# Performance work log

Measured on AMD Instinct MI355X. Metric: run time of the kernel, lower is better.

## Reference

```python
import jax, jax.numpy as jnp
import numpy as np

N = 50000      # nodes
E = 800000     # edges
FEAT = 128     # node_feat_size
HID = 128      # hidden_channels
LAT = 64       # latent_size
G = 256        # number of graphs in the batch


def _glorot_like(key, fan_in, shape):
    s = 1.0 / np.sqrt(fan_in)
    return jax.random.uniform(key, shape, jnp.float32, -s, s)


def setup_inputs() -> dict:
    key = jax.random.key(0)
    ks = jax.random.split(key, 13)
    x = jax.random.normal(ks[0], (N, FEAT), jnp.float32)
    edge_index = jax.random.randint(ks[1], (2, E), 0, N, dtype=jnp.int64)
    batch = jnp.sort(jax.random.randint(ks[2], (N,), 0, G, dtype=jnp.int64))
    return {
        "x": x,
        "edge_index": edge_index,
        "batch": batch,
        # GCNConv1: FEAT -> HID
        "W1": _glorot_like(ks[3], FEAT, (FEAT, HID)), "b1": jnp.zeros((HID,), jnp.float32),
        # GCNConv2: HID -> HID
        "W2": _glorot_like(ks[4], HID, (HID, HID)), "b2": jnp.zeros((HID,), jnp.float32),
        # fc: HID -> LAT
        "fcW": _glorot_like(ks[5], HID, (HID, LAT)), "fcb": _glorot_like(ks[6], HID, (LAT,)),
        # decoder: LAT -> HID
        "decW": _glorot_like(ks[7], LAT, (LAT, HID)), "decb": _glorot_like(ks[8], LAT, (HID,)),
        # GCNConv3: HID -> FEAT
        "W3": _glorot_like(ks[9], HID, (HID, FEAT)), "b3": jnp.zeros((FEAT,), jnp.float32),
    }


def reference(x, edge_index, batch, W1, b1, W2, b2, fcW, fcb, decW, decb, W3, b3):
    # --- GCN normalization with self-loops (computed once, shared by all convs) ---
    loop = jnp.arange(N, dtype=edge_index.dtype)
    row = jnp.concatenate([edge_index[0], loop])   # source nodes [E+N]
    col = jnp.concatenate([edge_index[1], loop])   # target nodes [E+N]
    deg = jax.ops.segment_sum(jnp.ones(row.shape, x.dtype), col, num_segments=N)
    dinv = jnp.where(deg > 0, jax.lax.rsqrt(deg), jnp.zeros_like(deg))
    norm = dinv[row] * dinv[col]                   # [E+N]

    def gcn(h, W, b):
        h = h @ W                                   # [N, out] transform first (PyG order)
        msg = h[row] * norm[:, None]                # gather + scale, [E+N, out]
        out = jax.ops.segment_sum(msg, col, num_segments=N)  # scatter-add
        return out + b

    # --- encode ---
    h = jax.nn.relu(gcn(x, W1, b1))
    h = jax.nn.relu(gcn(h, W2, b2))
    pooled = jax.ops.segment_sum(h, batch, num_segments=G)   # global_add_pool [G, HID]
    latent = jax.nn.relu(pooled @ fcW + fcb)                 # [G, LAT]

    # --- decode ---
    z = jax.nn.relu(latent @ decW + decb)                    # [G, HID]
    z = z[batch]                                             # broadcast back to nodes [N, HID]
    recon = gcn(z, W3, b3)                                   # [N, FEAT]
    return recon, latent
```

## Files before the change

kernel.cpp:

```cpp
#include <hip/hip_runtime.h>
#include <hip/hip_fp16.h>

static constexpr int NN   = 50000;
static constexpr int EE   = 800000;
static constexpr int GG   = 256;
static constexpr int PCH  = 16;
static constexpr int BK   = 128;
static constexpr int NB   = (NN + BK - 1) / BK;
static constexpr int CAP  = 4096;
static constexpr int CH   = 2048;
static constexpr int ABLK = (EE + CH - 1) / CH;

typedef _Float16 f16;
typedef f16  f16x8 __attribute__((ext_vector_type(8)));
typedef float f32x4 __attribute__((ext_vector_type(4)));

__device__ __forceinline__ int lowerb(const int* __restrict__ b, int n, int v) {
    int lo = 0, hi = n;
    while (lo < hi) { int m = (lo + hi) >> 1; if (b[m] < v) lo = m + 1; else hi = m; }
    return lo;
}

__global__ void init_k(int* __restrict__ bcur)
{
    int b = blockIdx.x * 256 + threadIdx.x;
    if (b < NB) bcur[b] = b * CAP;
}

__global__ __launch_bounds__(512) void binA_k(const int* __restrict__ ei,
                                              int* __restrict__ bcur,
                                              int2* __restrict__ eraw)
{
    __shared__ int2  stage[CH];
    __shared__ short sbid[CH];
    __shared__ int   hist[NB], loff[NB], gbase[NB], lcur[NB];
    __shared__ int   sc[512];

    int tid = threadIdx.x;
    int e0 = blockIdx.x * CH;
    int n = EE - e0; if (n > CH) n = CH;

    for (int b = tid; b < NB; b += 512) hist[b] = 0;
    __syncthreads();

    int2 r[CH / 512];
    #pragma unroll
    for (int k = 0; k < CH / 512; k++) {
        int s = k * 512 + tid;
        if (s < n) {
            int src = ei[e0 + s];
            int dst = ei[EE + e0 + s];
            r[k] = make_int2(src, dst);
            atomicAdd(&hist[dst >> 7], 1);
        }
    }
    __syncthreads();
    int v = (tid < NB) ? hist[tid] : 0;
    sc[tid] = v;
    __syncthreads();
    #pragma unroll
    for (int off = 1; off < 512; off <<= 1) {
        int add = (tid >= off) ? sc[tid - off] : 0;
        __syncthreads();
        sc[tid] += add;
        __syncthreads();
    }
    if (tid < NB) { int ex = sc[tid] - v; loff[tid] = ex; lcur[tid] = ex; }
    __syncthreads();
    for (int b = tid; b < NB; b += 512)
        gbase[b] = atomicAdd(&bcur[b], hist[b]);
    __syncthreads();
    #pragma unroll
    for (int k = 0; k < CH / 512; k++) {
        int s = k * 512 + tid;
        if (s < n) {
            int b = r[k].y >> 7;
            int slot = atomicAdd(&lcur[b], 1);
            stage[slot] = r[k];
            sbid[slot]  = (short)b;
        }
    }
    __syncthreads();
    for (int s = tid; s < n; s += 512) {
        int b = sbid[s];
        eraw[(size_t)gbase[b] + (s - loff[b])] = stage[s];
    }
}

__global__ __launch_bounds__(512) void scanb2_k(const int* __restrict__ bcur,
                                                int* __restrict__ bbase,
                                                int* __restrict__ rowptr)
{
    __shared__ int s[512];
    int t = threadIdx.x;
    int v = (t < NB) ? (bcur[t] - t * CAP) : 0;
    s[t] = v;
    __syncthreads();
    #pragma unroll
    for (int off = 1; off < 512; off <<= 1) {
        int add = (t >= off) ? s[t - off] : 0;
        __syncthreads();
        s[t] += add;
        __syncthreads();
    }
    if (t < NB) bbase[t] = s[t] - v;
    if (t == 0) rowptr[NN] = EE;
}

__global__ __launch_bounds__(512) void binB_k(const int2* __restrict__ eraw,
                                              const int* __restrict__ bcur,
                                              const int* __restrict__ bbase,
                                              int* __restrict__ rowptr,
                                              int* __restrict__ ebuf)
{
    __shared__ int hist[BK], excl[BK], cur[BK];
    int b = blockIdx.x, tid = threadIdx.x;
    int t0 = b << 7;
    int lim = NN - t0; if (lim > BK) lim = BK;
    int tot  = bcur[b] - b * CAP;
    int base = bbase[b];
    const int2* er = eraw + (size_t)b * CAP;

    if (tid < BK) hist[tid] = 0;
    __syncthreads();
    for (int s = tid; s < tot; s += 512) atomicAdd(&hist[er[s].y & 127], 1);
    __syncthreads();
    if (tid < BK) excl[tid] = hist[tid];
    __syncthreads();
    #pragma unroll
    for (int off = 1; off < BK; off <<= 1) {
        int add = (tid >= off && tid < BK) ? excl[tid - off] : 0;
        __syncthreads();
        if (tid < BK) excl[tid] += add;
        __syncthreads();
    }
    if (tid < BK) {
        int ex = excl[tid] - hist[tid];
        cur[tid] = base + ex;
        if (tid < lim) rowptr[t0 + tid] = base + ex;
    }
    __syncthreads();
    for (int s = tid; s < tot; s += 512) {
        int2 rec = er[s];
        int p = atomicAdd(&cur[rec.y & 127], 1);
        ebuf[p] = rec.x;
    }
}

__global__ void dinv_k(const int* __restrict__ rowptr, float* __restrict__ dinv)
{
    int i = blockIdx.x * 256 + threadIdx.x;
    if (i < NN) dinv[i] = rsqrtf((float)(rowptr[i + 1] - rowptr[i] + 1));
}

__global__ void pbb_k(const int* __restrict__ ebuf, const int* __restrict__ batch,
                      const float* __restrict__ dinv, int2* __restrict__ ebuf2)
{
    int e = blockIdx.x * 256 + threadIdx.x;
    if (e < EE) {
        int src = ebuf[e];
        ebuf2[e] = make_int2(batch[src], __float_as_int(dinv[src]));
    }
}

__global__ __launch_bounds__(256) void gemm_mfma_k(const float* __restrict__ in,
                                                   const float* __restrict__ W,
                                                   const float* __restrict__ dinv,
                                                   __half* __restrict__ out,
                                                   int rows)
{
    __shared__ __align__(16) f16 whi[128 * 128];
    __shared__ __align__(16) f16 wlo[128 * 128];

    int tid = threadIdx.x;
    {
        int n  = tid & 127;
        int kh = tid >> 7;
        int sw = (n & 7) << 4;
        #pragma unroll
        for (int jb = 0; jb < 8; jb++) {
            f16x8 h8, l8;
            #pragma unroll
            for (int u = 0; u < 8; u++) {
                int k = kh * 64 + jb * 8 + u;
                float x = W[k * 128 + n];
                f16 h = (f16)x;
                h8[u] = h;
                l8[u] = (f16)(x - (float)h);
            }
            int boff = n * 256 + ((kh * 128 + jb * 16) ^ sw);
            *(f16x8*)((char*)whi + boff) = h8;
            *(f16x8*)((char*)wlo + boff) = l8;
        }
    }
    __syncthreads();

    int lane = tid & 63;
    int wv   = tid >> 6;
    int rB   = blockIdx.x * 64 + wv * 16;
    int m    = lane & 15;
    int kq   = lane >> 4;
    int r    = rB + m;
    int rr   = (r < rows) ? r : (rows - 1);

    f16x8 ahi[4], alo[4];
    const float* rp = in + (size_t)rr * 128 + kq * 8;
    #pragma unroll
    for (int ks = 0; ks < 4; ks++) {
        float4 p0 = *(const float4*)(rp + ks * 32);
        float4 p1 = *(const float4*)(rp + ks * 32 + 4);
        float xs[8] = {p0.x, p0.y, p0.z, p0.w, p1.x, p1.y, p1.z, p1.w};
        #pragma unroll
        for (int u = 0; u < 8; u++) {
            f16 h = (f16)xs[u];
            ahi[ks][u] = h;
            alo[ks][u] = (f16)(xs[u] - (float)h);
        }
    }

    f32x4 acc[8];
    #pragma unroll
    for (int n = 0; n < 8; n++) acc[n] = (f32x4){0.f, 0.f, 0.f, 0.f};

    #pragma unroll
    for (int nt = 0; nt < 8; nt++) {
        int nb   = nt * 16 + m;
        int sw   = (nb & 7) << 4;
        int rowb = nb * 256;
        #pragma unroll
        for (int ks = 0; ks < 4; ks++) {
            int off = rowb + (((ks * 64) + (kq * 16)) ^ sw);
            f16x8 bh = *(const f16x8*)((const char*)whi + off);
            f16x8 bl = *(const f16x8*)((const char*)wlo + off);
            acc[nt] = __builtin_amdgcn_mfma_f32_16x16x32_f16(ahi[ks], bh, acc[nt], 0, 0, 0);
            acc[nt] = __builtin_amdgcn_mfma_f32_16x16x32_f16(alo[ks], bh, acc[nt], 0, 0, 0);
            acc[nt] = __builtin_amdgcn_mfma_f32_16x16x32_f16(ahi[ks], bl, acc[nt], 0, 0, 0);
        }
    }

    int   orow[4];
    float dv[4];
    #pragma unroll
    for (int j = 0; j < 4; j++) {
        int gr = rB + kq * 4 + j;
        orow[j] = gr;
        dv[j]   = (gr < rows) ? dinv[gr] : 0.f;
    }
    #pragma unroll
    for (int nt = 0; nt < 8; nt++) {
        int c = nt * 16 + m;
        #pragma unroll
        for (int j = 0; j < 4; j++) {
            if (orow[j] < rows)
                out[(size_t)orow[j] * 128 + c] = __float2half(acc[nt][j] * dv[j]);
        }
    }
}

__global__ __launch_bounds__(64) void aggh_k(const __half* __restrict__ t,
                                             const int* __restrict__ rowptr,
                                             const int* __restrict__ ebuf,
                                             const float* __restrict__ dinv,
                                             const float* __restrict__ bias,
                                             float* __restrict__ out,
                                             int relu)
{
    int i = blockIdx.x;
    int f = threadIdx.x;
    const __half2* tp = (const __half2*)t;
    float2 v = __half22float2(tp[(size_t)i * 64 + f]);
    float a0 = v.x, a1 = v.y;
    int e0 = __builtin_amdgcn_readfirstlane(rowptr[i]);
    int e1 = __builtin_amdgcn_readfirstlane(rowptr[i + 1]);
    int e = e0;
    for (; e + 7 < e1; e += 8) {
        int s0 = ebuf[e],     s1 = ebuf[e + 1];
        int s2 = ebuf[e + 2], s3 = ebuf[e + 3];
        int s4 = ebuf[e + 4], s5 = ebuf[e + 5];
        int s6 = ebuf[e + 6], s7 = ebuf[e + 7];
        float2 w0 = __half22float2(tp[(size_t)s0 * 64 + f]);
        float2 w1 = __half22float2(tp[(size_t)s1 * 64 + f]);
        float2 w2 = __half22float2(tp[(size_t)s2 * 64 + f]);
        float2 w3 = __half22float2(tp[(size_t)s3 * 64 + f]);
        float2 w4 = __half22float2(tp[(size_t)s4 * 64 + f]);
        float2 w5 = __half22float2(tp[(size_t)s5 * 64 + f]);
        float2 w6 = __half22float2(tp[(size_t)s6 * 64 + f]);
        float2 w7 = __half22float2(tp[(size_t)s7 * 64 + f]);
        a0 += w0.x + w1.x + w2.x + w3.x + w4.x + w5.x + w6.x + w7.x;
        a1 += w0.y + w1.y + w2.y + w3.y + w4.y + w5.y + w6.y + w7.y;
    }
    for (; e < e1; e++) {
        float2 w = __half22float2(tp[(size_t)ebuf[e] * 64 + f]);
        a0 += w.x; a1 += w.y;
    }
    float di = dinv[i];
    float2 b = ((const float2*)bias)[f];
    a0 = di * a0 + b.x;
    a1 = di * a1 + b.y;
    if (relu) { a0 = fmaxf(a0, 0.f); a1 = fmaxf(a1, 0.f); }
    ((float2*)out)[(size_t)i * 64 + f] = make_float2(a0, a1);
}

__global__ __launch_bounds__(64) void agg_out_k(const float* __restrict__ zz,
                                                const int* __restrict__ batch,
                                                const int* __restrict__ rowptr,
                                                const int2* __restrict__ ebuf2,
                                                const float* __restrict__ dinv,
                                                const float* __restrict__ bias,
                                                float* __restrict__ out)
{
    int i = blockIdx.x;
    int f = threadIdx.x;
    const float2* zp = (const float2*)zz;
    float di = dinv[i];
    float2 v = zp[(size_t)batch[i] * 64 + f];
    float a0 = di * v.x, a1 = di * v.y;
    int e0 = rowptr[i], e1 = rowptr[i + 1];
    int e = e0;
    for (; e + 3 < e1; e += 4) {
        int2 r0 = ebuf2[e],     r1 = ebuf2[e + 1];
        int2 r2 = ebuf2[e + 2], r3 = ebuf2[e + 3];
        float2 w0 = zp[(size_t)r0.x * 64 + f];
        float2 w1 = zp[(size_t)r1.x * 64 + f];
        float2 w2 = zp[(size_t)r2.x * 64 + f];
        float2 w3 = zp[(size_t)r3.x * 64 + f];
        float n0 = __int_as_float(r0.y), n1 = __int_as_float(r1.y);
        float n2 = __int_as_float(r2.y), n3 = __int_as_float(r3.y);
        a0 += n0 * w0.x; a1 += n0 * w0.y;
        a0 += n1 * w1.x; a1 += n1 * w1.y;
        a0 += n2 * w2.x; a1 += n2 * w2.y;
        a0 += n3 * w3.x; a1 += n3 * w3.y;
    }
    for (; e < e1; e++) {
        int2 r = ebuf2[e];
        float nm = __int_as_float(r.y);
        float2 w = zp[(size_t)r.x * 64 + f];
        a0 += nm * w.x; a1 += nm * w.y;
    }
    float2 b = ((const float2*)bias)[f];
    a0 = di * a0 + b.x;
    a1 = di * a1 + b.y;
    ((float2*)out)[(size_t)i * 64 + f] = make_float2(a0, a1);
}

__global__ __launch_bounds__(128) void pool2_k(const float* __restrict__ h2,
                                               const int* __restrict__ batch,
                                               float* __restrict__ pooled)
{
    int g = blockIdx.x;
    int c = blockIdx.y;
    int f = threadIdx.x;
    int bs = lowerb(batch, NN, g);
    int be = lowerb(batch, NN, g + 1);
    int len = be - bs;
    int cs = bs + (int)(((long long)len * c) / PCH);
    int ce = bs + (int)(((long long)len * (c + 1)) / PCH);
    float a = 0.f;
    for (int i = cs; i < ce; i++) a += h2[(size_t)i * 128 + f];
    if (ce > cs) atomicAdd(&pooled[(size_t)g * 128 + f], a);
}

__global__ __launch_bounds__(64) void fc_k(const float* __restrict__ pooled,
                                           const float* __restrict__ fcW,
                                           const float* __restrict__ fcb,
                                           float* __restrict__ latentf,
                                           float* __restrict__ lat_out)
{
    int g = blockIdx.x, l = threadIdx.x;
    const float* p = pooled + (size_t)g * 128;
    float a = fcb[l];
    #pragma unroll 8
    for (int k = 0; k < 128; k++) a = fmaf(p[k], fcW[(size_t)k * 64 + l], a);
    a = fmaxf(a, 0.f);
    latentf[(size_t)g * 64 + l] = a;
    lat_out[(size_t)g * 64 + l] = a;
}

__global__ __launch_bounds__(128) void dec_k(const float* __restrict__ latentf,
                                             const float* __restrict__ decW,
                                             const float* __restrict__ decb,
                                             const float* __restrict__ W3,
                                             float* __restrict__ zz)
{
    __shared__ float zs[128];
    int g = blockIdx.x, c = threadIdx.x;
    const float* lat = latentf + (size_t)g * 64;
    {
        float a = decb[c];
        #pragma unroll 8
        for (int k = 0; k < 64; k++) a = fmaf(lat[k], decW[(size_t)k * 128 + c], a);
        zs[c] = fmaxf(a, 0.f);
    }
    __syncthreads();
    float o = 0.f;
    #pragma unroll 8
    for (int k = 0; k < 128; k++) o = fmaf(zs[k], W3[(size_t)k * 128 + c], o);
    zz[(size_t)g * 128 + c] = o;
}

extern "C" void kernel_launch(void* const* d_in, const int* in_sizes, int n_in,
                              void* d_out, int out_size, void* d_ws, size_t ws_size,
                              hipStream_t stream)
{
    const float* x     = (const float*)d_in[0];
    const int*   ei    = (const int*)d_in[1];
    const int*   batch = (const int*)d_in[2];
    const float* W1  = (const float*)d_in[3];
    const float* b1  = (const float*)d_in[4];
    const float* W2  = (const float*)d_in[5];
    const float* b2  = (const float*)d_in[6];
    const float* fcW = (const float*)d_in[7];
    const float* fcb = (const float*)d_in[8];
    const float* decW= (const float*)d_in[9];
    const float* decb= (const float*)d_in[10];
    const float* W3  = (const float*)d_in[11];
    const float* b3  = (const float*)d_in[12];

    char* ws = (char*)d_ws;
    size_t off = 0;
    auto alloc = [&](size_t bytes) -> char* {
        char* p = ws + off;
        off = (off + bytes + 255) & ~(size_t)255;
        return p;
    };
    float* dinv     = (float*)alloc((size_t)NN * 4);
    int*   rowptr   = (int*)alloc((size_t)(NN + 1) * 4);
    int*   bcur     = (int*)alloc((size_t)NB * 4);
    int*   bbase    = (int*)alloc((size_t)NB * 4);
    int*   ebuf     = (int*)alloc((size_t)EE * 4);
    float* pooled   = (float*)alloc((size_t)GG * 128 * 4);
    float* latentf  = (float*)alloc((size_t)GG * 64 * 4);
    float* zz       = (float*)alloc((size_t)GG * 128 * 4);
    __half* A       = (__half*)alloc((size_t)NN * 128 * 2);
    float* B        = (float*)alloc((size_t)NN * 128 * 4);
    int2*  eraw     = (int2*)B;
    int2*  ebuf2    = (int2*)A;

    float* recon_out = (float*)d_out;
    float* lat_out   = (float*)d_out + (size_t)NN * 128;

    hipMemsetAsync(pooled, 0, (size_t)GG * 128 * 4, stream);
    init_k<<<(NB + 255) / 256, 256, 0, stream>>>(bcur);
    binA_k<<<ABLK, 512, 0, stream>>>(ei, bcur, eraw);
    scanb2_k<<<1, 512, 0, stream>>>(bcur, bbase, rowptr);
    binB_k<<<NB, 512, 0, stream>>>(eraw, bcur, bbase, rowptr, ebuf);
    dinv_k<<<(NN + 255) / 256, 256, 0, stream>>>(rowptr, dinv);

    int gblk = (NN + 63) / 64;
    gemm_mfma_k<<<gblk, 256, 0, stream>>>(x, W1, dinv, A, NN);
    aggh_k<<<NN, 64, 0, stream>>>(A, rowptr, ebuf, dinv, b1, B, 1);
    gemm_mfma_k<<<gblk, 256, 0, stream>>>(B, W2, dinv, A, NN);
    aggh_k<<<NN, 64, 0, stream>>>(A, rowptr, ebuf, dinv, b2, B, 1);
    pbb_k<<<(EE + 255) / 256, 256, 0, stream>>>(ebuf, batch, dinv, ebuf2);
    pool2_k<<<dim3(GG, PCH), 128, 0, stream>>>(B, batch, pooled);
    fc_k<<<GG, 64, 0, stream>>>(pooled, fcW, fcb, latentf, lat_out);
    dec_k<<<GG, 128, 0, stream>>>(latentf, decW, decb, W3, zz);
    agg_out_k<<<NN, 64, 0, stream>>>(zz, batch, rowptr, ebuf2, dinv,
                                     b3, recon_out);
}
```

Measured before the change: 293.5 us.

## Precompute MFMA-ordered split-fp16 weights and split aggregation across two feature halves

Weight hi/lo fp16 splitting moves out of each GEMM block into a small prep kernel. That kernel writes the split weights to global memory in MFMA fragment order, so the GEMM reads them straight from global/L2 with no shared-memory staging or syncthreads. This removes 64KB of LDS per block, which allows higher occupancy, and removes the redundant per-block conversion. The aggregation kernel now launches twice as many blocks, each handling 64 of the 128 features with scalar half loads. This gives more parallelism but duplicates the edge-index reads and gathers with narrower 2-byte accesses.

```diff
diff --git a/kernel.cpp b/kernel.cpp
--- a/kernel.cpp
+++ b/kernel.cpp
@@ -163,38 +163,37 @@
     }
 }
 
-__global__ __launch_bounds__(256) void gemm_mfma_k(const float* __restrict__ in,
-                                                   const float* __restrict__ W,
-                                                   const float* __restrict__ dinv,
-                                                   __half* __restrict__ out,
-                                                   int rows)
-{
-    __shared__ __align__(16) f16 whi[128 * 128];
-    __shared__ __align__(16) f16 wlo[128 * 128];
-
-    int tid = threadIdx.x;
-    {
-        int n  = tid & 127;
-        int kh = tid >> 7;
-        int sw = (n & 7) << 4;
-        #pragma unroll
-        for (int jb = 0; jb < 8; jb++) {
-            f16x8 h8, l8;
-            #pragma unroll
-            for (int u = 0; u < 8; u++) {
-                int k = kh * 64 + jb * 8 + u;
-                float x = W[k * 128 + n];
-                f16 h = (f16)x;
-                h8[u] = h;
-                l8[u] = (f16)(x - (float)h);
-            }
-            int boff = n * 256 + ((kh * 128 + jb * 16) ^ sw);
-            *(f16x8*)((char*)whi + boff) = h8;
-            *(f16x8*)((char*)wlo + boff) = l8;
-        }
-    }
-    __syncthreads();
-
+__global__ __launch_bounds__(256) void wprep_k(const float* __restrict__ W,
+                                               f16x8* __restrict__ whi_f,
+                                               f16x8* __restrict__ wlo_f)
+{
+    int tid = blockIdx.x * 256 + threadIdx.x;
+    int m  = tid & 15;
+    int kq = (tid >> 4) & 3;
+    int ks = (tid >> 6) & 3;
+    int nt = tid >> 8;
+    int n  = nt * 16 + m;
+    int k0 = ks * 32 + kq * 8;
+    f16x8 h8, l8;
+    #pragma unroll
+    for (int u = 0; u < 8; u++) {
+        float x = W[(size_t)(k0 + u) * 128 + n];
+        f16 h = (f16)x;
+        h8[u] = h;
+        l8[u] = (f16)(x - (float)h);
+    }
+    whi_f[tid] = h8;
+    wlo_f[tid] = l8;
+}
+
+__global__ __launch_bounds__(256) void gemm_mfma2_k(const float* __restrict__ in,
+                                                    const f16x8* __restrict__ whi_f,
+                                                    const f16x8* __restrict__ wlo_f,
+                                                    const float* __restrict__ dinv,
+                                                    __half* __restrict__ out,
+                                                    int rows)
+{
+    int tid  = threadIdx.x;
     int lane = tid & 63;
     int wv   = tid >> 6;
     int rB   = blockIdx.x * 64 + wv * 16;
@@ -224,14 +223,11 @@
 
     #pragma unroll
     for (int nt = 0; nt < 8; nt++) {
-        int nb   = nt * 16 + m;
-        int sw   = (nb & 7) << 4;
-        int rowb = nb * 256;
         #pragma unroll
         for (int ks = 0; ks < 4; ks++) {
-            int off = rowb + (((ks * 64) + (kq * 16)) ^ sw);
-            f16x8 bh = *(const f16x8*)((const char*)whi + off);
-            f16x8 bl = *(const f16x8*)((const char*)wlo + off);
+            int idx = ((nt * 4 + ks) * 4 + kq) * 16 + m;
+            f16x8 bh = whi_f[idx];
+            f16x8 bl = wlo_f[idx];
             acc[nt] = __builtin_amdgcn_mfma_f32_16x16x32_f16(ahi[ks], bh, acc[nt], 0, 0, 0);
             acc[nt] = __builtin_amdgcn_mfma_f32_16x16x32_f16(alo[ks], bh, acc[nt], 0, 0, 0);
             acc[nt] = __builtin_amdgcn_mfma_f32_16x16x32_f16(ahi[ks], bl, acc[nt], 0, 0, 0);
@@ -265,11 +261,11 @@
                                              float* __restrict__ out,
                                              int relu)
 {
-    int i = blockIdx.x;
-    int f = threadIdx.x;
-    const __half2* tp = (const __half2*)t;
-    float2 v = __half22float2(tp[(size_t)i * 64 + f]);
-    float a0 = v.x, a1 = v.y;
+    int bid = blockIdx.x;
+    int i = bid, h = 0;
+    if (i >= NN) { i -= NN; h = 1; }
+    int f = (h << 6) | threadIdx.x;
+    float a = __half2float(t[(size_t)i * 128 + f]);
     int e0 = __builtin_amdgcn_readfirstlane(rowptr[i]);
     int e1 = __builtin_amdgcn_readfirstlane(rowptr[i + 1]);
     int e = e0;
@@ -278,27 +274,23 @@
         int s2 = ebuf[e + 2], s3 = ebuf[e + 3];
         int s4 = ebuf[e + 4], s5 = ebuf[e + 5];
         int s6 = ebuf[e + 6], s7 = ebuf[e + 7];
-        float2 w0 = __half22float2(tp[(size_t)s0 * 64 + f]);
-        float2 w1 = __half22float2(tp[(size_t)s1 * 64 + f]);
-        float2 w2 = __half22float2(tp[(size_t)s2 * 64 + f]);
-        float2 w3 = __half22float2(tp[(size_t)s3 * 64 + f]);
-        float2 w4 = __half22float2(tp[(size_t)s4 * 64 + f]);
-        float2 w5 = __half22float2(tp[(size_t)s5 * 64 + f]);
-        float2 w6 = __half22float2(tp[(size_t)s6 * 64 + f]);
-        float2 w7 = __half22float2(tp[(size_t)s7 * 64 + f]);
-        a0 += w0.x + w1.x + w2.x + w3.x + w4.x + w5.x + w6.x + w7.x;
-        a1 += w0.y + w1.y + w2.y + w3.y + w4.y + w5.y + w6.y + w7.y;
+        float w0 = __half2float(t[(size_t)s0 * 128 + f]);
+        float w1 = __half2float(t[(size_t)s1 * 128 + f]);
+        float w2 = __half2float(t[(size_t)s2 * 128 + f]);
+        float w3 = __half2float(t[(size_t)s3 * 128 + f]);
+        float w4 = __half2float(t[(size_t)s4 * 128 + f]);
+        float w5 = __half2float(t[(size_t)s5 * 128 + f]);
+        float w6 = __half2float(t[(size_t)s6 * 128 + f]);
+        float w7 = __half2float(t[(size_t)s7 * 128 + f]);
+        a += w0 + w1 + w2 + w3 + w4 + w5 + w6 + w7;
     }
     for (; e < e1; e++) {
-        float2 w = __half22float2(tp[(size_t)ebuf[e] * 64 + f]);
-        a0 += w.x; a1 += w.y;
+        a += __half2float(t[(size_t)ebuf[e] * 128 + f]);
     }
     float di = dinv[i];
-    float2 b = ((const float2*)bias)[f];
-    a0 = di * a0 + b.x;
-    a1 = di * a1 + b.y;
-    if (relu) { a0 = fmaxf(a0, 0.f); a1 = fmaxf(a1, 0.f); }
-    ((float2*)out)[(size_t)i * 64 + f] = make_float2(a0, a1);
+    a = di * a + bias[f];
+    if (relu) a = fmaxf(a, 0.f);
+    out[(size_t)i * 128 + f] = a;
 }
 
 __global__ __launch_bounds__(64) void agg_out_k(const float* __restrict__ zz,
@@ -431,6 +423,10 @@
     float* pooled   = (float*)alloc((size_t)GG * 128 * 4);
     float* latentf  = (float*)alloc((size_t)GG * 64 * 4);
     float* zz       = (float*)alloc((size_t)GG * 128 * 4);
+    f16x8* whi1     = (f16x8*)alloc(2048 * 16);
+    f16x8* wlo1     = (f16x8*)alloc(2048 * 16);
+    f16x8* whi2     = (f16x8*)alloc(2048 * 16);
+    f16x8* wlo2     = (f16x8*)alloc(2048 * 16);
     __half* A       = (__half*)alloc((size_t)NN * 128 * 2);
     float* B        = (float*)alloc((size_t)NN * 128 * 4);
     int2*  eraw     = (int2*)B;
@@ -445,12 +441,14 @@
     scanb2_k<<<1, 512, 0, stream>>>(bcur, bbase, rowptr);
     binB_k<<<NB, 512, 0, stream>>>(eraw, bcur, bbase, rowptr, ebuf);
     dinv_k<<<(NN + 255) / 256, 256, 0, stream>>>(rowptr, dinv);
+    wprep_k<<<8, 256, 0, stream>>>(W1, whi1, wlo1);
+    wprep_k<<<8, 256, 0, stream>>>(W2, whi2, wlo2);
 
     int gblk = (NN + 63) / 64;
-    gemm_mfma_k<<<gblk, 256, 0, stream>>>(x, W1, dinv, A, NN);
-    aggh_k<<<NN, 64, 0, stream>>>(A, rowptr, ebuf, dinv, b1, B, 1);
-    gemm_mfma_k<<<gblk, 256, 0, stream>>>(B, W2, dinv, A, NN);
-    aggh_k<<<NN, 64, 0, stream>>>(A, rowptr, ebuf, dinv, b2, B, 1);
+    gemm_mfma2_k<<<gblk, 256, 0, stream>>>(x, whi1, wlo1, dinv, A, NN);
+    aggh_k<<<2 * NN, 64, 0, stream>>>(A, rowptr, ebuf, dinv, b1, B, 1);
+    gemm_mfma2_k<<<gblk, 256, 0, stream>>>(B, whi2, wlo2, dinv, A, NN);
+    aggh_k<<<2 * NN, 64, 0, stream>>>(A, rowptr, ebuf, dinv, b2, B, 1);
     pbb_k<<<(EE + 255) / 256, 256, 0, stream>>>(ebuf, batch, dinv, ebuf2);
     pool2_k<<<dim3(GG, PCH), 128, 0, stream>>>(B, batch, pooled);
     fc_k<<<GG, 64, 0, stream>>>(pooled, fcW, fcb, latentf, lat_out);
```

Measured after the change: 321.1 us. +9.4%, slower.
